# Kernel optimization log

Measured on AMD Instinct MI355X. Metric: run time of the kernel, lower is better.

The kernel has to match this reference:

```python
import jax, jax.numpy as jnp
import numpy as np

WINDOW = 16      # window_size[0]
LANDM_H = 8      # closest_square_factors(64) = (8, 8)
LANDM_W = 8
MAX_VAL = 5.0
PINV_ITERS = 6


def activ(x):
    # ExpLinearAfterThreshold: exp(clamp(x, max=5)) + relu(x - 5)
    return jnp.exp(jnp.minimum(x, MAX_VAL)) + jax.nn.relu(x - MAX_VAL)


def pool_landmarks(x):
    # x: [B, H, N, d] with N = WINDOW*WINDOW.
    B, H, N, d = x.shape
    kh, kw = WINDOW // LANDM_H, WINDOW // LANDM_W
    x = x.reshape(B, H, LANDM_H, kh, LANDM_W, kw, d)
    return x.mean(axis=(3, 5)).reshape(B, H, LANDM_H * LANDM_W, d)  # [B, H, L, d]


def moore_penrose_pinv(x, iters=PINV_ITERS):
    # x: [B, H, L, L]
    abs_x = jnp.abs(x)
    col = abs_x.sum(axis=-1)
    row = abs_x.sum(axis=-2)
    z = jnp.swapaxes(x, -1, -2) / (jnp.max(col) * jnp.max(row) + 1e-15)
    I = jnp.eye(x.shape[-1], dtype=x.dtype)
    for _ in range(iters):
        xz = x @ z
        z = 0.25 * z @ (13.0 * I - xz @ (15.0 * I - xz @ (7.0 * I - xz)))
    return z


def setup_inputs() -> dict:
    key = jax.random.key(0)
    kq, kk, kv = jax.random.split(key, 3)
    shape = (256, 16, 256, 64)  # [B_, num_heads, window^2, head_dim]
    q = jax.random.normal(kq, shape, dtype=jnp.float32)
    k = jax.random.normal(kk, shape, dtype=jnp.float32)
    v = jax.random.normal(kv, shape, dtype=jnp.float32)
    return {"q": q, "k": k, "v": v}


def reference(q, k, v):
    # q, k, v: [B, H, N, d]
    q_m = pool_landmarks(q)  # [B, H, L, d]
    k_m = pool_landmarks(k)  # [B, H, L, d]

    temp = activ(jnp.einsum('bhld,bhmd->bhlm', q_m, k_m))   # [B, H, L, L]
    pinv = moore_penrose_pinv(temp, PINV_ITERS)              # [B, H, L, L]

    # kernel(q_m, k) @ [v | 1]  -> [B, H, L, d+1]
    v1 = jnp.concatenate([v, jnp.ones_like(v[..., :1])], axis=-1)
    kv = jnp.einsum('bhln,bhne->bhle', activ(jnp.einsum('bhld,bhnd->bhln', q_m, k)), v1)

    # kernel(q, k_m) @ pinv @ kv  -> [B, H, N, d+1]
    qk = activ(jnp.einsum('bhnd,bhld->bhnl', q, k_m))        # [B, H, N, L]
    prod = jnp.einsum('bhnl,bhle->bhne', qk @ pinv, kv)

    return prod[..., :-1] / (prod[..., -1:] + 1e-12)
```

## Files before the change

### kernel.cpp

```cpp
#include <hip/hip_runtime.h>
#include <math.h>


#define G_TOT 4096
#define TPB_R 256
#define TPB_M 512
typedef _Float16 f16;
typedef __attribute__((ext_vector_type(2))) _Float16 f16x2;
typedef __attribute__((ext_vector_type(4))) _Float16 f16x4;
typedef __attribute__((ext_vector_type(8))) _Float16 f16x8;
typedef __attribute__((ext_vector_type(4))) float f32x4;
typedef __attribute__((ext_vector_type(16))) float f32x16;

#define NPLANES 18
#define SMEM_BYTES (NPLANES * 4096 * 2 + 2 * 64 * 4)

#define LSCALE 2048.0f
#define LINV   (1.0f / 2048.0f)
#define ZS     1024.0f
#define ZINV   (1.0f / 1024.0f)

struct HL { f16 h, l; };
__device__ __forceinline__ HL split2(float v) {
    HL r;
    r.h = (f16)v;
    r.l = (f16)((v - (float)r.h) * LSCALE);
    return r;
}
__device__ __forceinline__ float join2(f16 h, f16 l) {
    return (float)h + (float)l * LINV;
}
__device__ __forceinline__ int swi(int r, int c) {
    return (r << 6) + (c ^ ((r & 7) << 3));
}
__device__ __forceinline__ float activ_f(float x) {
    return expf(fminf(x, 5.0f)) + fmaxf(x - 5.0f, 0.0f);
}
__device__ __forceinline__ void split_w(f16* Ph, f16* Pl, int r, int c, float v) {
    HL s = split2(v);
    const int o = swi(r, c);
    Ph[o] = s.h;
    Pl[o] = s.l;
}
__device__ __forceinline__ f16x2 mk2(f16 a, f16 b) { f16x2 r; r[0]=a; r[1]=b; return r; }
__device__ __forceinline__ f16x4 mk4(f16 a, f16 b, f16 c, f16 d) { f16x4 r; r[0]=a;r[1]=b;r[2]=c;r[3]=d; return r; }
__device__ __forceinline__ f32x4 z4() { f32x4 z = {0.f,0.f,0.f,0.f}; return z; }
__device__ __forceinline__ f32x16 z16() {
    f32x16 z;
#pragma unroll
    for (int i = 0; i < 16; ++i) z[i] = 0.f;
    return z;
}

__device__ __forceinline__ f32x4 mm16(const f16* __restrict__ Ah, const f16* __restrict__ Al,
                                      const f16* __restrict__ Bh, const f16* __restrict__ Bl,
                                      int arow, int brow, int kg, f32x4 acc) {
    const int abase = arow << 6, axor = (arow & 7) << 3;
    const int bbase = brow << 6, bxor = (brow & 7) << 3;
    f32x4 ax1 = z4(), ax2 = z4();
#pragma unroll
    for (int s = 0; s < 2; ++s) {
        const int k0 = (s << 5) + (kg << 3);
        const int ao = abase + (k0 ^ axor);
        const int bo = bbase + (k0 ^ bxor);
        f16x8 a_h = *(const f16x8*)(Ah + ao);
        f16x8 a_l = *(const f16x8*)(Al + ao);
        f16x8 b_h = *(const f16x8*)(Bh + bo);
        f16x8 b_l = *(const f16x8*)(Bl + bo);
        acc = __builtin_amdgcn_mfma_f32_16x16x32_f16(a_h, b_h, acc, 0, 0, 0);
        ax1 = __builtin_amdgcn_mfma_f32_16x16x32_f16(a_h, b_l, ax1, 0, 0, 0);
        ax2 = __builtin_amdgcn_mfma_f32_16x16x32_f16(a_l, b_h, ax2, 0, 0, 0);
    }
    acc += (ax1 + ax2) * LINV;
    return acc;
}

__device__ __forceinline__ f32x16 mm64q(const f16* __restrict__ Ah, const f16* __restrict__ Al,
                                        const f16* __restrict__ Bh, const f16* __restrict__ Bl,
                                        int lane, int wr, int wc, f32x16 acc) {
    const int cl = lane & 31, hh = lane >> 5;
    const int ar = (wr << 5) + cl, br = (wc << 5) + cl;
    const int abase = ar << 6, axor = (ar & 7) << 3;
    const int bbase = br << 6, bxor = (br & 7) << 3;
    f32x16 ax1 = z16();
    f32x16 ax2 = z16();
#pragma unroll
    for (int ks = 0; ks < 4; ++ks) {
        const int k0 = (ks << 4) + (hh << 3);
        const int ao = abase + (k0 ^ axor);
        const int bo = bbase + (k0 ^ bxor);
        f16x8 a_h = *(const f16x8*)(Ah + ao);
        f16x8 a_l = *(const f16x8*)(Al + ao);
        f16x8 b_h = *(const f16x8*)(Bh + bo);
        f16x8 b_l = *(const f16x8*)(Bl + bo);
        acc = __builtin_amdgcn_mfma_f32_32x32x16_f16(a_h, b_h, acc, 0, 0, 0);
        ax1 = __builtin_amdgcn_mfma_f32_32x32x16_f16(a_h, b_l, ax1, 0, 0, 0);
        ax2 = __builtin_amdgcn_mfma_f32_32x32x16_f16(a_l, b_h, ax2, 0, 0, 0);
    }
    acc += (ax1 + ax2) * LINV;
    return acc;
}

__device__ __forceinline__ void stage_rm512(const float* __restrict__ src,
                                            f16* Ph, f16* Pl, int t) {
#pragma unroll
    for (int i = 0; i < 2; ++i) {
        const int f = (i << 9) + t;
        const int r = f >> 4, c4 = (f & 15) << 2;
        float4 vv = *(const float4*)(src + (size_t)f * 4);
        const int o = swi(r, c4);
        HL s0 = split2(vv.x), s1 = split2(vv.y), s2 = split2(vv.z), s3 = split2(vv.w);
        *(f16x4*)(Ph + o) = mk4(s0.h, s1.h, s2.h, s3.h);
        *(f16x4*)(Pl + o) = mk4(s0.l, s1.l, s2.l, s3.l);
    }
}

__device__ __forceinline__ void stage_t512(const float* __restrict__ src,
                                           f16* Ph, f16* Pl, int t) {
    const int n0 = (t >> 4) << 1;
    const int e0 = (t & 15) << 2;
    const float* p = src + (size_t)n0 * 64 + e0;
    float4 v0 = *(const float4*)p;
    float4 v1 = *(const float4*)(p + 64);
    const float* a = (const float*)&v0;
    const float* b = (const float*)&v1;
#pragma unroll
    for (int j = 0; j < 4; ++j) {
        HL sa = split2(a[j]), sb = split2(b[j]);
        const int o = swi(e0 + j, n0);
        *(f16x2*)(Ph + o) = mk2(sa.h, sb.h);
        *(f16x2*)(Pl + o) = mk2(sa.l, sb.l);
    }
}

__device__ __forceinline__ void pool_global512(const float* __restrict__ src,
                                               f16* Ph, f16* Pl, int t) {
    const int L = t >> 3;
    const int d0 = (t & 7) << 3;
    const int tt = L >> 4, ll = L & 15;
    const int rb = ((ll >> 3) << 5) + ((ll & 7) << 1);
    const float* p = src + (size_t)((tt << 6) + rb) * 64 + d0;
    float4 a0 = *(const float4*)p;          float4 a1 = *(const float4*)(p + 4);
    float4 b0 = *(const float4*)(p + 64);   float4 b1 = *(const float4*)(p + 68);
    float4 c0 = *(const float4*)(p + 1024); float4 c1 = *(const float4*)(p + 1028);
    float4 d0_ = *(const float4*)(p + 1088);float4 d1 = *(const float4*)(p + 1092);
    HL s0 = split2(0.25f * (a0.x + b0.x + c0.x + d0_.x));
    HL s1 = split2(0.25f * (a0.y + b0.y + c0.y + d0_.y));
    HL s2 = split2(0.25f * (a0.z + b0.z + c0.z + d0_.z));
    HL s3 = split2(0.25f * (a0.w + b0.w + c0.w + d0_.w));
    HL s4 = split2(0.25f * (a1.x + b1.x + c1.x + d1.x));
    HL s5 = split2(0.25f * (a1.y + b1.y + c1.y + d1.y));
    HL s6 = split2(0.25f * (a1.z + b1.z + c1.z + d1.z));
    HL s7 = split2(0.25f * (a1.w + b1.w + c1.w + d1.w));
    const int o = swi(L, d0);
    *(f16x4*)(Ph + o)     = mk4(s0.h, s1.h, s2.h, s3.h);
    *(f16x4*)(Ph + o + 4) = mk4(s4.h, s5.h, s6.h, s7.h);
    *(f16x4*)(Pl + o)     = mk4(s0.l, s1.l, s2.l, s3.l);
    *(f16x4*)(Pl + o + 4) = mk4(s4.l, s5.l, s6.l, s7.l);
}

__device__ __forceinline__ void pool_lds512(const f16* Kh, const f16* Kl,
                                            f16* Ph, f16* Pl, int t, int tt) {
    const int ll = t >> 5, d0 = (t & 31) << 1;
    const int rb = ((ll >> 3) << 5) + ((ll & 7) << 1);
    float s0 = 0.f, s1 = 0.f;
#pragma unroll
    for (int rr = 0; rr < 4; ++rr) {
        const int r = rb + (rr & 1) + ((rr >> 1) << 4);
        const int o = swi(r, d0);
        f16x2 h = *(const f16x2*)(Kh + o);
        f16x2 l = *(const f16x2*)(Kl + o);
        s0 += join2(h[0], l[0]);
        s1 += join2(h[1], l[1]);
    }
    const int L = (tt << 4) + ll;
    HL p0 = split2(0.25f * s0), p1 = split2(0.25f * s1);
    const int o = swi(L, d0);
    *(f16x2*)(Ph + o) = mk2(p0.h, p1.h);
    *(f16x2*)(Pl + o) = mk2(p0.l, p1.l);
}

__device__ __forceinline__ void pool_global_r(const float* __restrict__ src,
                                              f16* Ph, f16* Pl, int t) {
    const int ll = t >> 4, d0 = (t & 15) << 2;
    const int rb = ((ll >> 3) << 5) + ((ll & 7) << 1);
#pragma unroll
    for (int tt = 0; tt < 4; ++tt) {
        const float* p = src + (size_t)((tt << 6) + rb) * 64 + d0;
        float4 a = *(const float4*)p;
        float4 b = *(const float4*)(p + 64);
        float4 c = *(const float4*)(p + 1024);
        float4 d = *(const float4*)(p + 1088);
        const int L = (tt << 4) + ll;
        split_w(Ph, Pl, L, d0 + 0, 0.25f * (a.x + b.x + c.x + d.x));
        split_w(Ph, Pl, L, d0 + 1, 0.25f * (a.y + b.y + c.y + d.y));
        split_w(Ph, Pl, L, d0 + 2, 0.25f * (a.z + b.z + c.z + d.z));
        split_w(Ph, Pl, L, d0 + 3, 0.25f * (a.w + b.w + c.w + d.w));
    }
}

#define WAVE_SUM32(v)            \
    v += __shfl_xor(v, 1);       \
    v += __shfl_xor(v, 2);       \
    v += __shfl_xor(v, 4);       \
    v += __shfl_xor(v, 8);       \
    v += __shfl_xor(v, 16);

__global__ void k_init(float* ws) {
    if (threadIdx.x < 2) ws[threadIdx.x] = 0.0f;
}

__global__ __launch_bounds__(TPB_R) void k_reduce(const float* __restrict__ q,
                                                  const float* __restrict__ k,
                                                  float* __restrict__ ws) {
    __shared__ f16 pls[4 * 4096];
    __shared__ float rowS[64], colS[64];
    const int t = threadIdx.x, g = blockIdx.x;
    const int lane = t & 63, wv = t >> 6, wr = wv >> 1, wc = wv & 1;
    const int cl = lane & 31, hh = lane >> 5;
    if (t < 64) rowS[t] = 0.f;
    else if (t < 128) colS[t - 64] = 0.f;
    pool_global_r(q + (size_t)g * 16384, pls, pls + 4096, t);
    pool_global_r(k + (size_t)g * 16384, pls + 8192, pls + 12288, t);
    __syncthreads();
    f32x16 a = mm64q(pls, pls + 4096, pls + 8192, pls + 12288, lane, wr, wc, z16());
    float colp = 0.f;
#pragma unroll
    for (int m = 0; m < 16; ++m) {
        float x = activ_f(a[m]);
        const int R = (wr << 5) + (m & 3) + ((m >> 2) << 3) + (hh << 2);
        float vs = x;
        WAVE_SUM32(vs)
        if (cl == 0) atomicAdd(&rowS[R], vs);
        colp += x;
    }
    colp += __shfl_xor(colp, 32);
    if (hh == 0) atomicAdd(&colS[(wc << 5) + cl], colp);
    __syncthreads();
    if (t < 64) {
        float vmx = rowS[t];
        for (int off = 1; off < 64; off <<= 1) vmx = fmaxf(vmx, __shfl_xor(vmx, off));
        if (t == 0) atomicMax((int*)ws, __float_as_int(vmx));
    } else if (t < 128) {
        float vmx = colS[t - 64];
        for (int off = 1; off < 64; off <<= 1) vmx = fmaxf(vmx, __shfl_xor(vmx, off));
        if (t == 64) atomicMax(((int*)ws) + 1, __float_as_int(vmx));
    }
}

__global__ __launch_bounds__(TPB_M) void k_main(const float* __restrict__ q,
                                                const float* __restrict__ k,
                                                const float* __restrict__ v,
                                                const float* __restrict__ ws,
                                                float* __restrict__ out) {
    extern __shared__ f16 smu[];
    float* kv1 = (float*)(smu + NPLANES * 4096);
    float* den = kv1 + 64;
    const int t = threadIdx.x, g = blockIdx.x;
    const int lane = t & 63, w = t >> 6;
    const int ti = w & 3, tj0 = (w >> 2) << 1;
    const int fr = lane & 15, kg = lane >> 4;
    const int arow = (ti << 4) + fr;
    const int brow0 = (tj0 << 4) + fr;
    const int brow1 = brow0 + 16;
    const int C0 = brow0, C1 = brow1;
    const float* Gq = q + (size_t)g * 16384;
    const float* Gk = k + (size_t)g * 16384;
    const float* Gv = v + (size_t)g * 16384;
    float* og = out + (size_t)g * 16384;

    f16* QMh = smu +  0 * 4096; f16* QMl = smu +  1 * 4096;
    f16* KMh = smu +  2 * 4096; f16* KMl = smu +  3 * 4096;
    f16* P4  = smu +  4 * 4096; f16* P5  = smu +  5 * 4096;
    f16* Zrh = smu +  6 * 4096; f16* Zrl = smu +  7 * 4096;
    f16* Zth = smu +  8 * 4096; f16* Ztl = smu +  9 * 4096;
    f16* PAh = smu + 10 * 4096; f16* PAl = smu + 11 * 4096;
    f16* PBh = smu + 12 * 4096; f16* PBl = smu + 13 * 4096;
    f16* KVh = smu + 14 * 4096; f16* KVl = smu + 15 * 4096;
    f16* T2h = smu + 16 * 4096; f16* T2l = smu + 17 * 4096;
    f16* oTh = QMh; f16* oTl = QMl;

    if (t < 64) kv1[t] = 0.f;
    pool_global512(Gq, QMh, QMl, t);
    __syncthreads();

    f32x4 kva0 = z4(), kva1 = z4();
    for (int tt = 0; tt < 4; ++tt) {
        stage_rm512(Gk + (size_t)tt * 4096, P4, P5, t);
        stage_t512 (Gv + (size_t)tt * 4096, PAh, PAl, t);
        __syncthreads();
        pool_lds512(P4, P5, KMh, KMl, t, tt);
        f32x4 s0 = mm16(QMh, QMl, P4, P5, arow, brow0, kg, z4());
        f32x4 s1 = mm16(QMh, QMl, P4, P5, arow, brow1, kg, z4());
#pragma unroll
        for (int m = 0; m < 4; ++m) {
            const int R = (ti << 4) + (kg << 2) + m;
            const float x0 = activ_f(s0[m]);
            const float x1 = activ_f(s1[m]);
            split_w(PBh, PBl, R, C0, x0);
            split_w(PBh, PBl, R, C1, x1);
            float vs = x0 + x1;
            vs += __shfl_xor(vs, 1); vs += __shfl_xor(vs, 2);
            vs += __shfl_xor(vs, 4); vs += __shfl_xor(vs, 8);
            if (fr == 0) atomicAdd(&kv1[R], vs);
        }
        __syncthreads();
        kva0 = mm16(PBh, PBl, PAh, PAl, arow, brow0, kg, kva0);
        kva1 = mm16(PBh, PBl, PAh, PAl, arow, brow1, kg, kva1);
        __syncthreads();
    }
#pragma unroll
    for (int m = 0; m < 4; ++m) {
        const int R = (ti << 4) + (kg << 2) + m;
        split_w(KVh, KVl, C0, R, kva0[m]);
        split_w(KVh, KVl, C1, R, kva1[m]);
    }

    {
        f32x4 x0 = mm16(QMh, QMl, KMh, KMl, arow, brow0, kg, z4());
        f32x4 x1 = mm16(QMh, QMl, KMh, KMl, arow, brow1, kg, z4());
#pragma unroll
        for (int m = 0; m < 4; ++m) {
            const int R = (ti << 4) + (kg << 2) + m;
            split_w(P4, P5, R, C0, activ_f(x0[m]));
            split_w(P4, P5, R, C1, activ_f(x1[m]));
        }
    }
    __syncthreads();

    {
        const float scale = ZS / (ws[0] * ws[1] + 1e-15f);
#pragma unroll
        for (int i = 0; i < 2; ++i) {
            const int bi = (i << 9) + t;
            const int r0 = (bi >> 5) << 1, c0 = (bi & 31) << 1;
            const int o00 = swi(r0, c0), o10 = swi(r0 + 1, c0);
            const float v00 = join2(P4[o00], P5[o00]) * scale;
            const float v01 = join2(P4[o00 + 1], P5[o00 + 1]) * scale;
            const float v10 = join2(P4[o10], P5[o10]) * scale;
            const float v11 = join2(P4[o10 + 1], P5[o10 + 1]) * scale;
            HL s00 = split2(v00), s01 = split2(v01), s10 = split2(v10), s11 = split2(v11);
            *(f16x2*)(Zth + o00) = mk2(s00.h, s01.h);
            *(f16x2*)(Ztl + o00) = mk2(s00.l, s01.l);
            *(f16x2*)(Zth + o10) = mk2(s10.h, s11.h);
            *(f16x2*)(Ztl + o10) = mk2(s10.l, s11.l);
            const int p0 = swi(c0, r0), p1 = swi(c0 + 1, r0);
            *(f16x2*)(Zrh + p0) = mk2(s00.h, s10.h);
            *(f16x2*)(Zrl + p0) = mk2(s00.l, s10.l);
            *(f16x2*)(Zrh + p1) = mk2(s01.h, s11.h);
            *(f16x2*)(Zrl + p1) = mk2(s01.l, s11.l);
        }
    }
    __syncthreads();

    for (int it = 0; it < 6; ++it) {
        f32x4 a0 = mm16(P4, P5, Zth, Ztl, arow, brow0, kg, z4());
        f32x4 a1 = mm16(P4, P5, Zth, Ztl, arow, brow1, kg, z4());
#pragma unroll
        for (int m = 0; m < 4; ++m) {
            const int R = (ti << 4) + (kg << 2) + m;
            const float t10 = a0[m] * ZINV, t11 = a1[m] * ZINV;
            split_w(PAh, PAl, R, C0, t10);
            split_w(PAh, PAl, R, C1, t11);
            split_w(PBh, PBl, C0, R, t10);
            split_w(PBh, PBl, C1, R, t11);
        }
        __syncthreads();
        f32x4 b0 = mm16(PAh, PAl, PBh, PBl, arow, brow0, kg, z4());
        f32x4 b1 = mm16(PAh, PAl, PBh, PBl, arow, brow1, kg, z4());
#pragma unroll
        for (int m = 0; m < 4; ++m) {
            const int R = (ti << 4) + (kg << 2) + m;
            split_w(T2h, T2l, R, C0, b0[m]);
            split_w(T2h, T2l, R, C1, b1[m]);
        }
        __syncthreads();
        f32x4 c0a = mm16(T2h, T2l, PBh, PBl, arow, brow0, kg, z4());
        f32x4 c1a = mm16(T2h, T2l, PBh, PBl, arow, brow1, kg, z4());
#pragma unroll
        for (int m = 0; m < 4; ++m) {
            const int R = (ti << 4) + (kg << 2) + m;
#pragma unroll
            for (int tile = 0; tile < 2; ++tile) {
                const int C = tile ? C1 : C0;
                const int o = swi(R, C);
                const float t1 = join2(PAh[o], PAl[o]);
                const float t2 = join2(T2h[o], T2l[o]);
                const float t4 = tile ? c1a[m] : c0a[m];
                const float ov = ((R == C) ? 13.f : 0.f) - 15.f * t1 + 7.f * t2 - t4;
                split_w(oTh, oTl, C, R, ov);
            }
        }
        __syncthreads();
        f32x4 d0 = mm16(Zrh, Zrl, oTh, oTl, arow, brow0, kg, z4());
        f32x4 d1 = mm16(Zrh, Zrl, oTh, oTl, arow, brow1, kg, z4());
        __syncthreads();
#pragma unroll
        for (int m = 0; m < 4; ++m) {
            const int R = (ti << 4) + (kg << 2) + m;
            const float z0 = 0.25f * d0[m], z1 = 0.25f * d1[m];
            split_w(Zrh, Zrl, R, C0, z0);
            split_w(Zrh, Zrl, R, C1, z1);
            split_w(Zth, Ztl, C0, R, z0);
            split_w(Zth, Ztl, C1, R, z1);
        }
        __syncthreads();
    }

    const float kvC0 = kv1[C0];
    const float kvC1 = kv1[C1];
    for (int tt = 0; tt < 4; ++tt) {
        if (t < 64) den[t] = 0.f;
        stage_rm512(Gq + (size_t)tt * 4096, P4, P5, t);
        __syncthreads();
        f32x4 q0 = mm16(P4, P5, KMh, KMl, arow, brow0, kg, z4());
        f32x4 q1 = mm16(P4, P5, KMh, KMl, arow, brow1, kg, z4());
#pragma unroll
        for (int m = 0; m < 4; ++m) {
            const int R = (ti << 4) + (kg << 2) + m;
            split_w(PBh, PBl, R, C0, activ_f(q0[m]));
            split_w(PBh, PBl, R, C1, activ_f(q1[m]));
        }
        __syncthreads();
        f32x4 w0 = mm16(PBh, PBl, Zth, Ztl, arow, brow0, kg, z4());
        f32x4 w1 = mm16(PBh, PBl, Zth, Ztl, arow, brow1, kg, z4());
#pragma unroll
        for (int m = 0; m < 4; ++m) {
            const int R = (ti << 4) + (kg << 2) + m;
            const float wv0 = w0[m] * ZINV, wv1 = w1[m] * ZINV;
            split_w(PAh, PAl, R, C0, wv0);
            split_w(PAh, PAl, R, C1, wv1);
            float d_ = wv0 * kvC0 + wv1 * kvC1;
            d_ += __shfl_xor(d_, 1); d_ += __shfl_xor(d_, 2);
            d_ += __shfl_xor(d_, 4); d_ += __shfl_xor(d_, 8);
            if (fr == 0) atomicAdd(&den[R], d_);
        }
        __syncthreads();
        f32x4 p0 = mm16(PAh, PAl, KVh, KVl, arow, brow0, kg, z4());
        f32x4 p1 = mm16(PAh, PAl, KVh, KVl, arow, brow1, kg, z4());
#pragma unroll
        for (int m = 0; m < 4; ++m) {
            const int R = (ti << 4) + (kg << 2) + m;
            const float inv = 1.0f / (den[R] + 1e-12f);
            og[(size_t)((tt << 6) + R) * 64 + C0] = p0[m] * inv;
            og[(size_t)((tt << 6) + R) * 64 + C1] = p1[m] * inv;
        }
        __syncthreads();
    }
}

extern "C" void kernel_launch(void* const* d_in, const int* in_sizes, int n_in,
                              void* d_out, int out_size, void* d_ws, size_t ws_size,
                              hipStream_t stream) {
    const float* q = (const float*)d_in[0];
    const float* k = (const float*)d_in[1];
    const float* v = (const float*)d_in[2];
    float* out = (float*)d_out;
    float* ws  = (float*)d_ws;
    (void)in_sizes; (void)n_in; (void)out_size; (void)ws_size;

    hipFuncSetAttribute((const void*)k_main,
                        hipFuncAttributeMaxDynamicSharedMemorySize, SMEM_BYTES);

    k_init<<<1, 64, 0, stream>>>(ws);
    k_reduce<<<G_TOT, TPB_R, 0, stream>>>(q, k, ws);
    k_main<<<G_TOT, TPB_M, SMEM_BYTES, stream>>>(q, k, v, ws, out);
}
```

Before: 931.7 us.

## Double block size to one 16x16 tile per wave and prefetch K/V/Q into registers

Raises the main kernel to 1024 threads, so each of the 16 waves owns a single 16x16 output tile instead of two, and restructures the staging, pooling and epilogue loops to match. The next chunk of K, V and Q is loaded into registers before the current one is processed, overlapping global loads with MFMA work. This adds parallelism per block for a latency-bound per-window pipeline, at the cost of more barrier participants and higher register pressure under launch_bounds(1024,4).

```diff
diff --git a/kernel.cpp b/kernel.cpp
--- a/kernel.cpp
+++ b/kernel.cpp
@@ -4,7 +4,7 @@
 
 #define G_TOT 4096
 #define TPB_R 256
-#define TPB_M 512
+#define TPB_M 1024
 typedef _Float16 f16;
 typedef __attribute__((ext_vector_type(2))) _Float16 f16x2;
 typedef __attribute__((ext_vector_type(4))) _Float16 f16x4;
@@ -101,62 +101,45 @@
     return acc;
 }
 
-__device__ __forceinline__ void stage_rm512(const float* __restrict__ src,
-                                            f16* Ph, f16* Pl, int t) {
-#pragma unroll
-    for (int i = 0; i < 2; ++i) {
-        const int f = (i << 9) + t;
-        const int r = f >> 4, c4 = (f & 15) << 2;
-        float4 vv = *(const float4*)(src + (size_t)f * 4);
-        const int o = swi(r, c4);
-        HL s0 = split2(vv.x), s1 = split2(vv.y), s2 = split2(vv.z), s3 = split2(vv.w);
-        *(f16x4*)(Ph + o) = mk4(s0.h, s1.h, s2.h, s3.h);
-        *(f16x4*)(Pl + o) = mk4(s0.l, s1.l, s2.l, s3.l);
-    }
-}
-
-__device__ __forceinline__ void stage_t512(const float* __restrict__ src,
-                                           f16* Ph, f16* Pl, int t) {
-    const int n0 = (t >> 4) << 1;
-    const int e0 = (t & 15) << 2;
-    const float* p = src + (size_t)n0 * 64 + e0;
-    float4 v0 = *(const float4*)p;
-    float4 v1 = *(const float4*)(p + 64);
-    const float* a = (const float*)&v0;
-    const float* b = (const float*)&v1;
-#pragma unroll
-    for (int j = 0; j < 4; ++j) {
-        HL sa = split2(a[j]), sb = split2(b[j]);
-        const int o = swi(e0 + j, n0);
-        *(f16x2*)(Ph + o) = mk2(sa.h, sb.h);
-        *(f16x2*)(Pl + o) = mk2(sa.l, sb.l);
-    }
-}
-
-__device__ __forceinline__ void pool_global512(const float* __restrict__ src,
-                                               f16* Ph, f16* Pl, int t) {
-    const int L = t >> 3;
-    const int d0 = (t & 7) << 3;
-    const int tt = L >> 4, ll = L & 15;
-    const int rb = ((ll >> 3) << 5) + ((ll & 7) << 1);
-    const float* p = src + (size_t)((tt << 6) + rb) * 64 + d0;
-    float4 a0 = *(const float4*)p;          float4 a1 = *(const float4*)(p + 4);
-    float4 b0 = *(const float4*)(p + 64);   float4 b1 = *(const float4*)(p + 68);
-    float4 c0 = *(const float4*)(p + 1024); float4 c1 = *(const float4*)(p + 1028);
-    float4 d0_ = *(const float4*)(p + 1088);float4 d1 = *(const float4*)(p + 1092);
-    HL s0 = split2(0.25f * (a0.x + b0.x + c0.x + d0_.x));
-    HL s1 = split2(0.25f * (a0.y + b0.y + c0.y + d0_.y));
-    HL s2 = split2(0.25f * (a0.z + b0.z + c0.z + d0_.z));
-    HL s3 = split2(0.25f * (a0.w + b0.w + c0.w + d0_.w));
-    HL s4 = split2(0.25f * (a1.x + b1.x + c1.x + d1.x));
-    HL s5 = split2(0.25f * (a1.y + b1.y + c1.y + d1.y));
-    HL s6 = split2(0.25f * (a1.z + b1.z + c1.z + d1.z));
-    HL s7 = split2(0.25f * (a1.w + b1.w + c1.w + d1.w));
+__device__ __forceinline__ void wr_rm(float4 vv, f16* Ph, f16* Pl, int t) {
+    const int r = t >> 4, c4 = (t & 15) << 2;
+    const int o = swi(r, c4);
+    HL s0 = split2(vv.x), s1 = split2(vv.y), s2 = split2(vv.z), s3 = split2(vv.w);
+    *(f16x4*)(Ph + o) = mk4(s0.h, s1.h, s2.h, s3.h);
+    *(f16x4*)(Pl + o) = mk4(s0.l, s1.l, s2.l, s3.l);
+}
+__device__ __forceinline__ void ld_vt(const float* __restrict__ src, int t,
+                                      float2& va, float2& vb) {
+    const int n0 = (t >> 5) << 1, e0 = (t & 31) << 1;
+    va = *(const float2*)(src + (size_t)n0 * 64 + e0);
+    vb = *(const float2*)(src + (size_t)(n0 + 1) * 64 + e0);
+}
+__device__ __forceinline__ void wr_vt(float2 va, float2 vb, f16* Ph, f16* Pl, int t) {
+    const int n0 = (t >> 5) << 1, e0 = (t & 31) << 1;
+    HL ax = split2(va.x), ay = split2(va.y), bx = split2(vb.x), by = split2(vb.y);
+    const int o0 = swi(e0, n0), o1 = swi(e0 + 1, n0);
+    *(f16x2*)(Ph + o0) = mk2(ax.h, bx.h);
+    *(f16x2*)(Pl + o0) = mk2(ax.l, bx.l);
+    *(f16x2*)(Ph + o1) = mk2(ay.h, by.h);
+    *(f16x2*)(Pl + o1) = mk2(ay.l, by.l);
+}
+
+__device__ __forceinline__ void pool_global1024(const float* __restrict__ src,
+                                                f16* Ph, f16* Pl, int t) {
+    const int L = t >> 4, d0 = (t & 15) << 2;
+    const int nb = ((L >> 3) << 5) + ((L & 7) << 1);
+    const float* p = src + (size_t)nb * 64 + d0;
+    float4 a = *(const float4*)p;
+    float4 b = *(const float4*)(p + 64);
+    float4 c = *(const float4*)(p + 1024);
+    float4 d = *(const float4*)(p + 1088);
+    HL s0 = split2(0.25f * (a.x + b.x + c.x + d.x));
+    HL s1 = split2(0.25f * (a.y + b.y + c.y + d.y));
+    HL s2 = split2(0.25f * (a.z + b.z + c.z + d.z));
+    HL s3 = split2(0.25f * (a.w + b.w + c.w + d.w));
     const int o = swi(L, d0);
-    *(f16x4*)(Ph + o)     = mk4(s0.h, s1.h, s2.h, s3.h);
-    *(f16x4*)(Ph + o + 4) = mk4(s4.h, s5.h, s6.h, s7.h);
-    *(f16x4*)(Pl + o)     = mk4(s0.l, s1.l, s2.l, s3.l);
-    *(f16x4*)(Pl + o + 4) = mk4(s4.l, s5.l, s6.l, s7.l);
+    *(f16x4*)(Ph + o) = mk4(s0.h, s1.h, s2.h, s3.h);
+    *(f16x4*)(Pl + o) = mk4(s0.l, s1.l, s2.l, s3.l);
 }
 
 __device__ __forceinline__ void pool_lds512(const f16* Kh, const f16* Kl,
@@ -248,22 +231,22 @@
     }
 }
 
-__global__ __launch_bounds__(TPB_M) void k_main(const float* __restrict__ q,
-                                                const float* __restrict__ k,
-                                                const float* __restrict__ v,
-                                                const float* __restrict__ ws,
-                                                float* __restrict__ out) {
+__global__ __launch_bounds__(TPB_M, 4) void k_main(const float* __restrict__ q,
+                                                   const float* __restrict__ k,
+                                                   const float* __restrict__ v,
+                                                   const float* __restrict__ ws,
+                                                   float* __restrict__ out) {
     extern __shared__ f16 smu[];
     float* kv1 = (float*)(smu + NPLANES * 4096);
     float* den = kv1 + 64;
     const int t = threadIdx.x, g = blockIdx.x;
     const int lane = t & 63, w = t >> 6;
-    const int ti = w & 3, tj0 = (w >> 2) << 1;
+    const int ti = w & 3, tj = w >> 2;
     const int fr = lane & 15, kg = lane >> 4;
     const int arow = (ti << 4) + fr;
-    const int brow0 = (tj0 << 4) + fr;
-    const int brow1 = brow0 + 16;
-    const int C0 = brow0, C1 = brow1;
+    const int brow = (tj << 4) + fr;
+    const int C = brow;
+    const int Rb = (ti << 4) + (kg << 2);
     const float* Gq = q + (size_t)g * 16384;
     const float* Gk = k + (size_t)g * 16384;
     const float* Gv = v + (size_t)g * 16384;
@@ -281,169 +264,134 @@
     f16* oTh = QMh; f16* oTl = QMl;
 
     if (t < 64) kv1[t] = 0.f;
-    pool_global512(Gq, QMh, QMl, t);
+    pool_global1024(Gq, QMh, QMl, t);
     __syncthreads();
 
-    f32x4 kva0 = z4(), kva1 = z4();
+    f32x4 kva = z4();
+    float4 kreg = *(const float4*)(Gk + (size_t)t * 4);
+    float2 va, vb;
+    ld_vt(Gv, t, va, vb);
     for (int tt = 0; tt < 4; ++tt) {
-        stage_rm512(Gk + (size_t)tt * 4096, P4, P5, t);
-        stage_t512 (Gv + (size_t)tt * 4096, PAh, PAl, t);
-        __syncthreads();
-        pool_lds512(P4, P5, KMh, KMl, t, tt);
-        f32x4 s0 = mm16(QMh, QMl, P4, P5, arow, brow0, kg, z4());
-        f32x4 s1 = mm16(QMh, QMl, P4, P5, arow, brow1, kg, z4());
-#pragma unroll
-        for (int m = 0; m < 4; ++m) {
-            const int R = (ti << 4) + (kg << 2) + m;
-            const float x0 = activ_f(s0[m]);
-            const float x1 = activ_f(s1[m]);
-            split_w(PBh, PBl, R, C0, x0);
-            split_w(PBh, PBl, R, C1, x1);
-            float vs = x0 + x1;
+        wr_rm(kreg, P4, P5, t);
+        wr_vt(va, vb, PAh, PAl, t);
+        if (tt < 3) {
+            kreg = *(const float4*)(Gk + (size_t)(tt + 1) * 4096 + (size_t)t * 4);
+            ld_vt(Gv + (size_t)(tt + 1) * 4096, t, va, vb);
+        }
+        __syncthreads();
+        if (t < 512) pool_lds512(P4, P5, KMh, KMl, t, tt);
+        f32x4 s = mm16(QMh, QMl, P4, P5, arow, brow, kg, z4());
+#pragma unroll
+        for (int m = 0; m < 4; ++m) {
+            const int R = Rb + m;
+            const float x = activ_f(s[m]);
+            split_w(PBh, PBl, R, C, x);
+            float vs = x;
             vs += __shfl_xor(vs, 1); vs += __shfl_xor(vs, 2);
             vs += __shfl_xor(vs, 4); vs += __shfl_xor(vs, 8);
             if (fr == 0) atomicAdd(&kv1[R], vs);
         }
         __syncthreads();
-        kva0 = mm16(PBh, PBl, PAh, PAl, arow, brow0, kg, kva0);
-        kva1 = mm16(PBh, PBl, PAh, PAl, arow, brow1, kg, kva1);
-        __syncthreads();
-    }
-#pragma unroll
-    for (int m = 0; m < 4; ++m) {
-        const int R = (ti << 4) + (kg << 2) + m;
-        split_w(KVh, KVl, C0, R, kva0[m]);
-        split_w(KVh, KVl, C1, R, kva1[m]);
-    }
+        kva = mm16(PBh, PBl, PAh, PAl, arow, brow, kg, kva);
+        __syncthreads();
+    }
+#pragma unroll
+    for (int m = 0; m < 4; ++m) split_w(KVh, KVl, C, Rb + m, kva[m]);
 
     {
-        f32x4 x0 = mm16(QMh, QMl, KMh, KMl, arow, brow0, kg, z4());
-        f32x4 x1 = mm16(QMh, QMl, KMh, KMl, arow, brow1, kg, z4());
-#pragma unroll
-        for (int m = 0; m < 4; ++m) {
-            const int R = (ti << 4) + (kg << 2) + m;
-            split_w(P4, P5, R, C0, activ_f(x0[m]));
-            split_w(P4, P5, R, C1, activ_f(x1[m]));
-        }
+        f32x4 x0 = mm16(QMh, QMl, KMh, KMl, arow, brow, kg, z4());
+#pragma unroll
+        for (int m = 0; m < 4; ++m) split_w(P4, P5, Rb + m, C, activ_f(x0[m]));
     }
     __syncthreads();
 
     {
         const float scale = ZS / (ws[0] * ws[1] + 1e-15f);
-#pragma unroll
-        for (int i = 0; i < 2; ++i) {
-            const int bi = (i << 9) + t;
-            const int r0 = (bi >> 5) << 1, c0 = (bi & 31) << 1;
-            const int o00 = swi(r0, c0), o10 = swi(r0 + 1, c0);
-            const float v00 = join2(P4[o00], P5[o00]) * scale;
-            const float v01 = join2(P4[o00 + 1], P5[o00 + 1]) * scale;
-            const float v10 = join2(P4[o10], P5[o10]) * scale;
-            const float v11 = join2(P4[o10 + 1], P5[o10 + 1]) * scale;
-            HL s00 = split2(v00), s01 = split2(v01), s10 = split2(v10), s11 = split2(v11);
-            *(f16x2*)(Zth + o00) = mk2(s00.h, s01.h);
-            *(f16x2*)(Ztl + o00) = mk2(s00.l, s01.l);
-            *(f16x2*)(Zth + o10) = mk2(s10.h, s11.h);
-            *(f16x2*)(Ztl + o10) = mk2(s10.l, s11.l);
-            const int p0 = swi(c0, r0), p1 = swi(c0 + 1, r0);
-            *(f16x2*)(Zrh + p0) = mk2(s00.h, s10.h);
-            *(f16x2*)(Zrl + p0) = mk2(s00.l, s10.l);
-            *(f16x2*)(Zrh + p1) = mk2(s01.h, s11.h);
-            *(f16x2*)(Zrl + p1) = mk2(s01.l, s11.l);
-        }
+        const int r0 = (t >> 5) << 1, c0 = (t & 31) << 1;
+        const int o00 = swi(r0, c0), o10 = swi(r0 + 1, c0);
+        const float v00 = join2(P4[o00], P5[o00]) * scale;
+        const float v01 = join2(P4[o00 + 1], P5[o00 + 1]) * scale;
+        const float v10 = join2(P4[o10], P5[o10]) * scale;
+        const float v11 = join2(P4[o10 + 1], P5[o10 + 1]) * scale;
+        HL s00 = split2(v00), s01 = split2(v01), s10 = split2(v10), s11 = split2(v11);
+        *(f16x2*)(Zth + o00) = mk2(s00.h, s01.h);
+        *(f16x2*)(Ztl + o00) = mk2(s00.l, s01.l);
+        *(f16x2*)(Zth + o10) = mk2(s10.h, s11.h);
+        *(f16x2*)(Ztl + o10) = mk2(s10.l, s11.l);
+        const int p0 = swi(c0, r0), p1 = swi(c0 + 1, r0);
+        *(f16x2*)(Zrh + p0) = mk2(s00.h, s10.h);
+        *(f16x2*)(Zrl + p0) = mk2(s00.l, s10.l);
+        *(f16x2*)(Zrh + p1) = mk2(s01.h, s11.h);
+        *(f16x2*)(Zrl + p1) = mk2(s01.l, s11.l);
     }
     __syncthreads();
 
     for (int it = 0; it < 6; ++it) {
-        f32x4 a0 = mm16(P4, P5, Zth, Ztl, arow, brow0, kg, z4());
-        f32x4 a1 = mm16(P4, P5, Zth, Ztl, arow, brow1, kg, z4());
-#pragma unroll
-        for (int m = 0; m < 4; ++m) {
-            const int R = (ti << 4) + (kg << 2) + m;
-            const float t10 = a0[m] * ZINV, t11 = a1[m] * ZINV;
-            split_w(PAh, PAl, R, C0, t10);
-            split_w(PAh, PAl, R, C1, t11);
-            split_w(PBh, PBl, C0, R, t10);
-            split_w(PBh, PBl, C1, R, t11);
-        }
-        __syncthreads();
-        f32x4 b0 = mm16(PAh, PAl, PBh, PBl, arow, brow0, kg, z4());
-        f32x4 b1 = mm16(PAh, PAl, PBh, PBl, arow, brow1, kg, z4());
-#pragma unroll
-        for (int m = 0; m < 4; ++m) {
-            const int R = (ti << 4) + (kg << 2) + m;
-            split_w(T2h, T2l, R, C0, b0[m]);
-            split_w(T2h, T2l, R, C1, b1[m]);
-        }
-        __syncthreads();
-        f32x4 c0a = mm16(T2h, T2l, PBh, PBl, arow, brow0, kg, z4());
-        f32x4 c1a = mm16(T2h, T2l, PBh, PBl, arow, brow1, kg, z4());
-#pragma unroll
-        for (int m = 0; m < 4; ++m) {
-            const int R = (ti << 4) + (kg << 2) + m;
-#pragma unroll
-            for (int tile = 0; tile < 2; ++tile) {
-                const int C = tile ? C1 : C0;
-                const int o = swi(R, C);
-                const float t1 = join2(PAh[o], PAl[o]);
-                const float t2 = join2(T2h[o], T2l[o]);
-                const float t4 = tile ? c1a[m] : c0a[m];
-                const float ov = ((R == C) ? 13.f : 0.f) - 15.f * t1 + 7.f * t2 - t4;
-                split_w(oTh, oTl, C, R, ov);
-            }
-        }
-        __syncthreads();
-        f32x4 d0 = mm16(Zrh, Zrl, oTh, oTl, arow, brow0, kg, z4());
-        f32x4 d1 = mm16(Zrh, Zrl, oTh, oTl, arow, brow1, kg, z4());
-        __syncthreads();
-#pragma unroll
-        for (int m = 0; m < 4; ++m) {
-            const int R = (ti << 4) + (kg << 2) + m;
-            const float z0 = 0.25f * d0[m], z1 = 0.25f * d1[m];
-            split_w(Zrh, Zrl, R, C0, z0);
-            split_w(Zrh, Zrl, R, C1, z1);
-            split_w(Zth, Ztl, C0, R, z0);
-            split_w(Zth, Ztl, C1, R, z1);
-        }
-        __syncthreads();
-    }
-
-    const float kvC0 = kv1[C0];
-    const float kvC1 = kv1[C1];
+        f32x4 a0 = mm16(P4, P5, Zth, Ztl, arow, brow, kg, z4());
+#pragma unroll
+        for (int m = 0; m < 4; ++m) {
+            const int R = Rb + m;
+            const float t1 = a0[m] * ZINV;
+            split_w(PAh, PAl, R, C, t1);
+            split_w(PBh, PBl, C, R, t1);
+        }
+        __syncthreads();
+        f32x4 b0 = mm16(PAh, PAl, PBh, PBl, arow, brow, kg, z4());
+#pragma unroll
+        for (int m = 0; m < 4; ++m) split_w(T2h, T2l, Rb + m, C, b0[m]);
+        __syncthreads();
+        f32x4 c0a = mm16(T2h, T2l, PBh, PBl, arow, brow, kg, z4());
+#pragma unroll
+        for (int m = 0; m < 4; ++m) {
+            const int R = Rb + m;
+            const int o = swi(R, C);
+            const float t1 = join2(PAh[o], PAl[o]);
+            const float t2 = join2(T2h[o], T2l[o]);
+            const float ov = ((R == C) ? 13.f : 0.f) - 15.f * t1 + 7.f * t2 - c0a[m];
+            split_w(oTh, oTl, C, R, ov);
+        }
+        __syncthreads();
+        f32x4 d0 = mm16(Zrh, Zrl, oTh, oTl, arow, brow, kg, z4());
+        __syncthreads();
+#pragma unroll
+        for (int m = 0; m < 4; ++m) {
+            const int R = Rb + m;
+            const float z0 = 0.25f * d0[m];
+            split_w(Zrh, Zrl, R, C, z0);
+            split_w(Zth, Ztl, C, R, z0);
+        }
+        __syncthreads();
+    }
+
+    const float kvC = kv1[C];
+    float4 qreg = *(const float4*)(Gq + (size_t)t * 4);
     for (int tt = 0; tt < 4; ++tt) {
         if (t < 64) den[t] = 0.f;
-        stage_rm512(Gq + (size_t)tt * 4096, P4, P5, t);
-        __syncthreads();
-        f32x4 q0 = mm16(P4, P5, KMh, KMl, arow, brow0, kg, z4());
-        f32x4 q1 = mm16(P4, P5, KMh, KMl, arow, brow1, kg, z4());
-#pragma unroll
-        for (int m = 0; m < 4; ++m) {
-            const int R = (ti << 4) + (kg << 2) + m;
-            split_w(PBh, PBl, R, C0, activ_f(q0[m]));
-            split_w(PBh, PBl, R, C1, activ_f(q1[m]));
-        }
-        __syncthreads();
-        f32x4 w0 = mm16(PBh, PBl, Zth, Ztl, arow, brow0, kg, z4());
-        f32x4 w1 = mm16(PBh, PBl, Zth, Ztl, arow, brow1, kg, z4());
-#pragma unroll
-        for (int m = 0; m < 4; ++m) {
-            const int R = (ti << 4) + (kg << 2) + m;
-            const float wv0 = w0[m] * ZINV, wv1 = w1[m] * ZINV;
-            split_w(PAh, PAl, R, C0, wv0);
-            split_w(PAh, PAl, R, C1, wv1);
-            float d_ = wv0 * kvC0 + wv1 * kvC1;
+        wr_rm(qreg, P4, P5, t);
+        if (tt < 3) qreg = *(const float4*)(Gq + (size_t)(tt + 1) * 4096 + (size_t)t * 4);
+        __syncthreads();
+        f32x4 q0 = mm16(P4, P5, KMh, KMl, arow, brow, kg, z4());
+#pragma unroll
+        for (int m = 0; m < 4; ++m) split_w(PBh, PBl, Rb + m, C, activ_f(q0[m]));
+        __syncthreads();
+        f32x4 w0 = mm16(PBh, PBl, Zth, Ztl, arow, brow, kg, z4());
+#pragma unroll
+        for (int m = 0; m < 4; ++m) {
+            const int R = Rb + m;
+            const float wv = w0[m] * ZINV;
+            split_w(PAh, PAl, R, C, wv);
+            float d_ = wv * kvC;
             d_ += __shfl_xor(d_, 1); d_ += __shfl_xor(d_, 2);
             d_ += __shfl_xor(d_, 4); d_ += __shfl_xor(d_, 8);
             if (fr == 0) atomicAdd(&den[R], d_);
         }
         __syncthreads();
-        f32x4 p0 = mm16(PAh, PAl, KVh, KVl, arow, brow0, kg, z4());
-        f32x4 p1 = mm16(PAh, PAl, KVh, KVl, arow, brow1, kg, z4());
-#pragma unroll
-        for (int m = 0; m < 4; ++m) {
-            const int R = (ti << 4) + (kg << 2) + m;
+        f32x4 p0 = mm16(PAh, PAl, KVh, KVl, arow, brow, kg, z4());
+#pragma unroll
+        for (int m = 0; m < 4; ++m) {
+            const int R = Rb + m;
             const float inv = 1.0f / (den[R] + 1e-12f);
-            og[(size_t)((tt << 6) + R) * 64 + C0] = p0[m] * inv;
-            og[(size_t)((tt << 6) + R) * 64 + C1] = p1[m] * inv;
+            og[(size_t)((tt << 6) + R) * 64 + C] = p0[m] * inv;
         }
         __syncthreads();
     }
```

Measured after the change: 909.0 us. -2.4%, faster.
